# Kernel optimization log

Hardware: AMD Instinct MI355X
Metric: run time of the kernel (lower is better)

## Reference

```python
import jax, jax.numpy as jnp
import numpy as np

NUM_HEADS = 16
HEAD_DIM = 80
HIDDEN = 1280
SEQ = 3072
NUM_SEGS = 6  # 6 packed images of 512 patches each


def rotate_half(x):
    x1, x2 = jnp.split(x, 2, axis=-1)
    return jnp.concatenate([-x2, x1], axis=-1)


def setup_inputs() -> dict:
    key = jax.random.key(0)
    ks = jax.random.split(key, 6)
    hidden_states = jax.random.normal(ks[0], (SEQ, HIDDEN), dtype=jnp.float32)
    # RoPE tables as in Qwen-VL vision: freqs over half the head_dim, duplicated
    half = HEAD_DIM // 2
    inv_freq = 1.0 / (10000.0 ** (jnp.arange(half, dtype=jnp.float32) / half))
    pos = jnp.arange(SEQ, dtype=jnp.float32)[:, None]
    freqs = pos * inv_freq[None, :]                      # (SEQ, half)
    emb = jnp.concatenate([freqs, freqs], axis=-1)       # (SEQ, HEAD_DIM)
    cos = jnp.cos(emb)
    sin = jnp.sin(emb)
    # Packed segment boundaries: [0, 512, 1024, ..., 3072]
    cu_seqlens = jnp.arange(0, SEQ + 1, SEQ // NUM_SEGS, dtype=jnp.int32)
    scale = 0.02
    w_qkv = jax.random.normal(ks[1], (3 * HIDDEN, HIDDEN), dtype=jnp.float32) * scale
    b_qkv = jax.random.normal(ks[2], (3 * HIDDEN,), dtype=jnp.float32) * scale
    w_proj = jax.random.normal(ks[3], (HIDDEN, HIDDEN), dtype=jnp.float32) * scale
    b_proj = jax.random.normal(ks[4], (HIDDEN,), dtype=jnp.float32) * scale
    return {
        "hidden_states": hidden_states, "cos": cos, "sin": sin,
        "w_qkv": w_qkv, "b_qkv": b_qkv, "w_proj": w_proj, "b_proj": b_proj,
        "cu_seqlens": cu_seqlens,
    }


def reference(hidden_states, cos, sin, w_qkv, b_qkv, w_proj, b_proj, cu_seqlens):
    S, H = hidden_states.shape
    nh, hd = NUM_HEADS, H // NUM_HEADS

    # Fused QKV projection: (S, 3H) -> q, k, v each (S, nh, hd)
    qkv = hidden_states @ w_qkv.T + b_qkv
    qkv = qkv.reshape(S, 3, nh, hd)
    q, k, v = qkv[:, 0], qkv[:, 1], qkv[:, 2]

    # Inline RoPE on q/k (cos/sin broadcast over heads)
    c = cos[:, None, :]
    s = sin[:, None, :]
    q = q * c + rotate_half(q) * s
    k = k * c + rotate_half(k) * s

    # Original casts fp32 -> fp16 for the flash attention kernel
    q16 = q.astype(jnp.float16)
    k16 = k.astype(jnp.float16)
    v16 = v.astype(jnp.float16)

    # Varlen masking: tokens attend only within their own packed segment
    tok = jnp.arange(S)
    seg = jnp.searchsorted(cu_seqlens, tok, side="right")  # (S,)
    same_seg = seg[:, None] == seg[None, :]                 # (S, S)

    scale = hd ** (-0.5)
    # Scores accumulated in fp32 (as flash attention does internally)
    scores = jnp.einsum("qhd,khd->hqk", q16, k16,
                        preferred_element_type=jnp.float32) * scale
    scores = jnp.where(same_seg[None], scores, jnp.finfo(jnp.float32).min)
    weights = jax.nn.softmax(scores, axis=-1).astype(jnp.float16)  # (nh, S, S)

    attn = jnp.einsum("hqk,khd->qhd", weights, v16)  # (S, nh, hd) fp16
    attn = attn.astype(jnp.float32).reshape(S, H)
    return attn @ w_proj.T + b_proj
```

## Files before the change

### kernel.cpp

```cpp
#include <hip/hip_runtime.h>

typedef _Float16 f16;
typedef _Float16 half8 __attribute__((ext_vector_type(8)));
typedef _Float16 half4 __attribute__((ext_vector_type(4)));
typedef float f32x4 __attribute__((ext_vector_type(4)));

__device__ __forceinline__ void gld_lds16(const void* g, void* l) {
  __builtin_amdgcn_global_load_lds((const __attribute__((address_space(1))) void*)g,
                                   (__attribute__((address_space(3))) void*)l, 16, 0, 0);
}

template <int CTRL>
__device__ __forceinline__ float dppf(float x) {
  return __builtin_bit_cast(float,
      __builtin_amdgcn_mov_dpp(__builtin_bit_cast(int, x), CTRL, 0xf, 0xf, true));
}
__device__ __forceinline__ float dpp_max16(float v) {
  v = fmaxf(v, dppf<0xB1>(v));
  v = fmaxf(v, dppf<0x4E>(v));
  v = fmaxf(v, dppf<0x128>(v));
  v = fmaxf(v, dppf<0x140>(v));
  return v;
}
__device__ __forceinline__ float dpp_sum16(float v) {
  v += dppf<0xB1>(v);
  v += dppf<0x4E>(v);
  v += dppf<0x128>(v);
  v += dppf<0x140>(v);
  return v;
}

__global__ void cvt_all(const float* __restrict__ hid, const float* __restrict__ wq,
                        const float* __restrict__ wp, f16* __restrict__ hid16,
                        f16* __restrict__ wq16, f16* __restrict__ wp16) {
  int b = blockIdx.x;
  const float* in;
  f16* out;
  int i;
  if (b < 3840) { in = hid; out = hid16; i = b * 256 + threadIdx.x; }
  else if (b < 8640) { in = wq; out = wq16; i = (b - 3840) * 256 + threadIdx.x; }
  else { in = wp; out = wp16; i = (b - 8640) * 256 + threadIdx.x; }
  float4 v = ((const float4*)in)[i];
  half4 o;
  o.x = (f16)v.x; o.y = (f16)v.y; o.z = (f16)v.z; o.w = (f16)v.w;
  ((half4*)out)[i] = o;
}

__global__ __launch_bounds__(512, 2) void gemm240(const f16* __restrict__ A,
                                                  const f16* __restrict__ B,
                                                  const float* __restrict__ bias,
                                                  f16* __restrict__ C) {
  __shared__ f16 S[57344];
  char* Sb = (char*)S;
  const int tid = threadIdx.x, lane = tid & 63, wid = tid >> 6;
  const int lm = lane & 15, q4 = lane >> 4;
  const int wm = wid >> 2, wn = wid & 3;
  const int swz = ((int)blockIdx.x & 7) * 30 + ((int)blockIdx.x >> 3);
  const int bm = (swz % 12) * 256, bn = (swz / 12) * 192;

  const int ch = ((lane & 7) ^ (lane >> 3)) << 3;
  uint32_t aoff[4], boff[3];
#pragma unroll
  for (int q = 0; q < 4; q++)
    aoff[q] = (uint32_t)((bm + q * 64 + wid * 8 + (lane >> 3)) * 1280 + ch);
#pragma unroll
  for (int i = 0; i < 3; i++)
    boff[i] = (uint32_t)((bn + wid * 24 + i * 8 + (lane >> 3)) * 1280 + ch);

  const int xr = (lm & 7) << 4;
  int aro[2][2], bro[3][2];
#pragma unroll
  for (int f = 0; f < 2; f++)
#pragma unroll
    for (int ks = 0; ks < 2; ks++)
      aro[f][ks] = (wm * 32 + f * 16 + lm) * 128 + ((ks * 64 + q4 * 16) ^ xr);
#pragma unroll
  for (int nh = 0; nh < 3; nh++)
#pragma unroll
    for (int ks = 0; ks < 2; ks++)
      bro[nh][ks] = (nh * 64 + wn * 16 + lm) * 128 + ((ks * 64 + q4 * 16) ^ xr);

  f32x4 acc[8][3] = {};

  {
#pragma unroll
    for (int q = 0; q < 4; q++)
      gld_lds16(A + aoff[q], Sb + q * 8192 + wid * 1024);
#pragma unroll
    for (int i = 0; i < 3; i++)
      gld_lds16(B + boff[i], Sb + 65536 + (3 * wid + i) * 1024);
#pragma unroll
    for (int i = 0; i < 3; i++)
      gld_lds16(B + boff[i] + 64, Sb + 65536 + 24576 + (3 * wid + i) * 1024);
#pragma unroll
    for (int q = 0; q < 3; q++)
      gld_lds16(A + aoff[q] + 64, Sb + 32768 + q * 8192 + wid * 1024);
    asm volatile("s_waitcnt vmcnt(6)" ::: "memory");
    __builtin_amdgcn_s_barrier();
  }

  constexpr int NT = 20;
  half8 af[2][2], bf[3][2];
  for (int t = 0; t < NT; ++t) {
    const int p = t & 1;
    char* Ab = Sb + p * 32768;
    char* Bb = Sb + 65536 + p * 24576;
    const int k1 = (t + 1 < NT ? t + 1 : NT - 1) * 64;
    const int k2 = (t + 2 < NT ? t + 2 : NT - 1) * 64;

#pragma unroll
    for (int f = 0; f < 2; f++) {
      af[f][0] = *(const half8*)(Ab + aro[f][0]);
      af[f][1] = *(const half8*)(Ab + aro[f][1]);
    }
#pragma unroll
    for (int nh = 0; nh < 3; nh++) {
      bf[nh][0] = *(const half8*)(Bb + bro[nh][0]);
      bf[nh][1] = *(const half8*)(Bb + bro[nh][1]);
    }
    gld_lds16(A + aoff[3] + k1, Sb + (p ^ 1) * 32768 + 3 * 8192 + wid * 1024);
    __builtin_amdgcn_s_barrier();
    asm volatile("s_waitcnt lgkmcnt(0)" ::: "memory");
    __builtin_amdgcn_sched_barrier(0);
    __builtin_amdgcn_s_setprio(1);
#pragma unroll
    for (int ks = 0; ks < 2; ks++)
#pragma unroll
      for (int f = 0; f < 2; f++)
#pragma unroll
        for (int nh = 0; nh < 3; nh++)
          acc[f][nh] =
              __builtin_amdgcn_mfma_f32_16x16x32_f16(af[f][ks], bf[nh][ks], acc[f][nh], 0, 0, 0);
    __builtin_amdgcn_s_setprio(0);
    __builtin_amdgcn_s_barrier();

#pragma unroll
    for (int f = 0; f < 2; f++) {
      af[f][0] = *(const half8*)(Ab + 8192 + aro[f][0]);
      af[f][1] = *(const half8*)(Ab + 8192 + aro[f][1]);
    }
#pragma unroll
    for (int i = 0; i < 3; i++)
      gld_lds16(B + boff[i] + k2, Bb + (3 * wid + i) * 1024);
    gld_lds16(A + aoff[0] + k2, Ab + wid * 1024);
    __builtin_amdgcn_s_barrier();
    asm volatile("s_waitcnt lgkmcnt(0)" ::: "memory");
    __builtin_amdgcn_sched_barrier(0);
    __builtin_amdgcn_s_setprio(1);
#pragma unroll
    for (int ks = 0; ks < 2; ks++)
#pragma unroll
      for (int f = 0; f < 2; f++)
#pragma unroll
        for (int nh = 0; nh < 3; nh++)
          acc[2 + f][nh] = __builtin_amdgcn_mfma_f32_16x16x32_f16(af[f][ks], bf[nh][ks],
                                                                  acc[2 + f][nh], 0, 0, 0);
    __builtin_amdgcn_s_setprio(0);
    __builtin_amdgcn_s_barrier();

#pragma unroll
    for (int f = 0; f < 2; f++) {
      af[f][0] = *(const half8*)(Ab + 16384 + aro[f][0]);
      af[f][1] = *(const half8*)(Ab + 16384 + aro[f][1]);
    }
    gld_lds16(A + aoff[1] + k2, Ab + 8192 + wid * 1024);
    __builtin_amdgcn_s_barrier();
    asm volatile("s_waitcnt lgkmcnt(0)" ::: "memory");
    __builtin_amdgcn_sched_barrier(0);
    __builtin_amdgcn_s_setprio(1);
#pragma unroll
    for (int ks = 0; ks < 2; ks++)
#pragma unroll
      for (int f = 0; f < 2; f++)
#pragma unroll
        for (int nh = 0; nh < 3; nh++)
          acc[4 + f][nh] = __builtin_amdgcn_mfma_f32_16x16x32_f16(af[f][ks], bf[nh][ks],
                                                                  acc[4 + f][nh], 0, 0, 0);
    __builtin_amdgcn_s_setprio(0);
    __builtin_amdgcn_s_barrier();

#pragma unroll
    for (int f = 0; f < 2; f++) {
      af[f][0] = *(const half8*)(Ab + 24576 + aro[f][0]);
      af[f][1] = *(const half8*)(Ab + 24576 + aro[f][1]);
    }
    gld_lds16(A + aoff[2] + k2, Ab + 16384 + wid * 1024);
    asm volatile("s_waitcnt vmcnt(6)" ::: "memory");
    __builtin_amdgcn_s_barrier();
    asm volatile("s_waitcnt lgkmcnt(0)" ::: "memory");
    __builtin_amdgcn_sched_barrier(0);
    __builtin_amdgcn_s_setprio(1);
#pragma unroll
    for (int ks = 0; ks < 2; ks++)
#pragma unroll
      for (int f = 0; f < 2; f++)
#pragma unroll
        for (int nh = 0; nh < 3; nh++)
          acc[6 + f][nh] = __builtin_amdgcn_mfma_f32_16x16x32_f16(af[f][ks], bf[nh][ks],
                                                                  acc[6 + f][nh], 0, 0, 0);
    __builtin_amdgcn_s_setprio(0);
    __builtin_amdgcn_s_barrier();
  }

#pragma unroll
  for (int mf = 0; mf < 8; mf++)
#pragma unroll
    for (int nf = 0; nf < 3; nf++) {
      const int gc = bn + nf * 64 + wn * 16 + lm;
      const float bb = bias[gc];
      const int gr0 = bm + (mf >> 1) * 64 + wm * 32 + (mf & 1) * 16 + q4 * 4;
#pragma unroll
      for (int r = 0; r < 4; r++)
        C[(size_t)(gr0 + r) * 3840 + gc] = (f16)(acc[mf][nf][r] + bb);
    }
}

template <bool OUT_F16>
__global__ __launch_bounds__(256, 2) void gemm_bt64(const f16* __restrict__ A,
                                                    const f16* __restrict__ B,
                                                    const float* __restrict__ bias,
                                                    void* __restrict__ Cout,
                                                    int K, int lda, int ldb, int ldc) {
  __shared__ f16 As[64 * 32];
  __shared__ f16 Bs[128 * 32];
  const int tid = threadIdx.x, lane = tid & 63, wave = tid >> 6;
  const int bm = blockIdx.x * 64, bn = blockIdx.y * 128;
  const int wm = (wave & 1) * 32, wn = (wave >> 1) * 64;
  const int lm = lane & 15, kq = (lane >> 4) * 8;
  const int arow = tid >> 2, acol = (tid & 3) * 8;

  const f16* Ab = A + (size_t)(bm + arow) * lda + acol;
  const f16* Bb = B + (size_t)(bn + arow) * ldb + acol;
  f16* AsW = As + wave * 512;
  f16* BsW = Bs + wave * 512;

  f32x4 acc[2][4] = {};
  for (int k0 = 0; k0 < K; k0 += 32) {
    gld_lds16(Ab + k0, AsW);
    gld_lds16(Bb + k0, BsW);
    gld_lds16(Bb + (size_t)64 * ldb + k0, BsW + 2048);
    __syncthreads();
    half8 af[2], bf[4];
#pragma unroll
    for (int mt = 0; mt < 2; mt++) af[mt] = *(const half8*)&As[(wm + 16 * mt + lm) * 32 + kq];
#pragma unroll
    for (int nt = 0; nt < 4; nt++) bf[nt] = *(const half8*)&Bs[(wn + 16 * nt + lm) * 32 + kq];
#pragma unroll
    for (int mt = 0; mt < 2; mt++)
#pragma unroll
      for (int nt = 0; nt < 4; nt++)
        acc[mt][nt] = __builtin_amdgcn_mfma_f32_16x16x32_f16(af[mt], bf[nt], acc[mt][nt], 0, 0, 0);
    __syncthreads();
  }
  const int q4 = lane >> 4;
#pragma unroll
  for (int mt = 0; mt < 2; mt++)
#pragma unroll
    for (int nt = 0; nt < 4; nt++)
#pragma unroll
      for (int r = 0; r < 4; r++) {
        int gr = bm + wm + 16 * mt + 4 * q4 + r;
        int gc = bn + wn + 16 * nt + lm;
        float v = acc[mt][nt][r] + bias[gc];
        if (OUT_F16)
          ((f16*)Cout)[(size_t)gr * ldc + gc] = (f16)v;
        else
          ((float*)Cout)[(size_t)gr * ldc + gc] = v;
      }
}

__global__ void rope_transpose(f16* __restrict__ qkv, const float* __restrict__ cosb,
                               const float* __restrict__ sinb, f16* __restrict__ vt) {
  __shared__ f16 tile[64][72];
  const int b = blockIdx.x;
  if (b < 1920) {
    int idx = b * 256 + threadIdx.x;
    int c = idx % 5;
    int t = idx / 5;
    int h = t % 16; t /= 16;
    int qk = t & 1;
    int s = t >> 1;
    size_t base = (size_t)s * 3840 + qk * 1280 + h * 80 + c * 8;
    half8 x = *(half8*)&qkv[base];
    half8 y = *(half8*)&qkv[base + 40];
    const float* cp = cosb + s * 80 + c * 8;
    const float* sp = sinb + s * 80 + c * 8;
    half8 ox, oy;
#pragma unroll
    for (int i = 0; i < 8; i++) {
      float cs = cp[i], sn = sp[i];
      float xf = (float)x[i], yf = (float)y[i];
      ox[i] = (f16)(xf * cs - yf * sn);
      oy[i] = (f16)(yf * cs + xf * sn);
    }
    *(half8*)&qkv[base] = ox;
    *(half8*)&qkv[base + 40] = oy;
  } else {
    const int bb = b - 1920;
    const int bs = (bb % 48) * 64;
    const int bd = (bb / 48) * 64;
    const int r = threadIdx.x >> 2, c = (threadIdx.x & 3) * 16;
    *(uint4*)&tile[r][c] = *(const uint4*)&qkv[(size_t)(bs + r) * 3840 + 2560 + bd + c];
    *(uint4*)&tile[r][c + 8] = *(const uint4*)&qkv[(size_t)(bs + r) * 3840 + 2560 + bd + c + 8];
    __syncthreads();
    f16 tmp[16];
#pragma unroll
    for (int i = 0; i < 16; i++) tmp[i] = tile[c + i][r];
    *(uint4*)&vt[(size_t)(bd + r) * 3072 + bs + c] = *(uint4*)&tmp[0];
    *(uint4*)&vt[(size_t)(bd + r) * 3072 + bs + c + 8] = *(uint4*)&tmp[8];
  }
}

__global__ __launch_bounds__(256, 3) void flash_attn6(const f16* __restrict__ qkv,
                                                      const f16* __restrict__ vt,
                                                      f16* __restrict__ attn) {
  __shared__ f16 S[25088];
  const int tid = threadIdx.x, lane = tid & 63, wave = tid >> 6;
  const int lm = lane & 15, q4 = lane >> 4;
  const int h = blockIdx.x, g = blockIdx.z;
  const int qbase = g * 512 + blockIdx.y * 64 + wave * 16;
  f16* P = S + 20480 + wave * 1152;
  const half8 hz = {};

  const f16* qrow = qkv + (size_t)(qbase + lm) * 3840 + h * 80;
  half8 qf[3];
  qf[0] = *(const half8*)(qrow + q4 * 8);
  qf[1] = *(const half8*)(qrow + 32 + q4 * 8);
  qf[2] = (q4 < 2) ? *(const half8*)(qrow + 64 + q4 * 8) : hz;

  const bool isK = wave < 2;
  const f16* gsrc = isK ? qkv : vt;
  const uint32_t gstep = isK ? (uint32_t)(64 * 3840) : 64u;
  const int cbase = (wave & 1) * 5;
  const uint32_t ldsoff = (isK ? 0u : 5120u) + (uint32_t)cbase * 512u;
  uint32_t goff[5];
#pragma unroll
  for (int i = 0; i < 5; i++) {
    int t = (cbase + i) * 1024 + lane * 16;
    if (isK) {
      int row = t / 160, colb = t % 160;
      goff[i] = (uint32_t)((g * 512 + row) * 3840 + 1280 + h * 80 + (colb >> 1));
    } else {
      int vd = t >> 7, vsb = t & 127;
      int vsrc = vsb ^ ((vd & 7) << 4);
      goff[i] = (uint32_t)((h * 80 + vd) * 3072 + g * 512 + (vsrc >> 1));
    }
  }

  f32x4 oacc[5] = {};
  float mprev[4] = {-1e30f, -1e30f, -1e30f, -1e30f};
  float lsum[4] = {0.f, 0.f, 0.f, 0.f};
  const float sc = 0.11180339887498949f * 1.4426950408889634f;

#pragma unroll
  for (int i = 0; i < 5; i++) gld_lds16(gsrc + goff[i], S + ldsoff + i * 512);
  __syncthreads();

  for (int jj = 0; jj < 8; jj++) {
    const int p = jj & 1;
    f16* Kb = S + p * 10240;
    f16* Vb = Kb + 5120;
    if (jj < 7) {
#pragma unroll
      for (int i = 0; i < 5; i++)
        gld_lds16(gsrc + goff[i] + (uint32_t)(jj + 1) * gstep,
                  S + (p ^ 1) * 10240 + ldsoff + i * 512);
    }

    f32x4 sacc[4] = {};
#pragma unroll
    for (int ks = 0; ks < 3; ks++) {
      half8 bk[4];
#pragma unroll
      for (int nt = 0; nt < 4; nt++)
        bk[nt] = (ks < 2 || q4 < 2)
                     ? *(const half8*)&Kb[(16 * nt + lm) * 80 + 32 * ks + q4 * 8]
                     : hz;
#pragma unroll
      for (int nt = 0; nt < 4; nt++)
        sacc[nt] = __builtin_amdgcn_mfma_f32_16x16x32_f16(qf[ks], bk[nt], sacc[nt], 0, 0, 0);
    }

    float mnew[4], alpha[4], rs[4];
#pragma unroll
    for (int r = 0; r < 4; r++) {
      float v = fmaxf(fmaxf(sacc[0][r], sacc[1][r]), fmaxf(sacc[2][r], sacc[3][r]));
      v = dpp_max16(v);
      mnew[r] = fmaxf(mprev[r], v * sc);
      alpha[r] = __builtin_exp2f(mprev[r] - mnew[r]);
      mprev[r] = mnew[r];
      rs[r] = 0.f;
    }
#pragma unroll
    for (int nt = 0; nt < 4; nt++)
#pragma unroll
      for (int r = 0; r < 4; r++) {
        float pp = __builtin_exp2f(sacc[nt][r] * sc - mnew[r]);
        sacc[nt][r] = pp;
        rs[r] += pp;
      }
#pragma unroll
    for (int r = 0; r < 4; r++) {
      float v = dpp_sum16(rs[r]);
      lsum[r] = alpha[r] * lsum[r] + v;
#pragma unroll
      for (int nt2 = 0; nt2 < 5; nt2++) oacc[nt2][r] *= alpha[r];
    }

#pragma unroll
    for (int nt = 0; nt < 4; nt++)
#pragma unroll
      for (int r = 0; r < 4; r++)
        P[(4 * q4 + r) * 72 + 16 * nt + lm] = (f16)sacc[nt][r];

#pragma unroll
    for (int ks = 0; ks < 2; ks++) {
      half8 ap = *(const half8*)&P[lm * 72 + ks * 32 + q4 * 8];
      half8 bv[5];
#pragma unroll
      for (int nt2 = 0; nt2 < 5; nt2++) {
        int row = 16 * nt2 + lm;
        bv[nt2] = *(const half8*)&Vb[row * 64 + ((ks * 32 + q4 * 8) ^ ((row & 7) << 3))];
      }
#pragma unroll
      for (int nt2 = 0; nt2 < 5; nt2++)
        oacc[nt2] = __builtin_amdgcn_mfma_f32_16x16x32_f16(ap, bv[nt2], oacc[nt2], 0, 0, 0);
    }

    __syncthreads();
  }

#pragma unroll
  for (int r = 0; r < 4; r++) {
    float inv = 1.0f / lsum[r];
    int s = qbase + 4 * q4 + r;
#pragma unroll
    for (int nt2 = 0; nt2 < 5; nt2++)
      attn[(size_t)s * 1280 + h * 80 + 16 * nt2 + lm] = (f16)(oacc[nt2][r] * inv);
  }
}

extern "C" void kernel_launch(void* const* d_in, const int* in_sizes, int n_in,
                              void* d_out, int out_size, void* d_ws, size_t ws_size,
                              hipStream_t stream) {
  const float* hidden = (const float*)d_in[0];
  const float* cosb   = (const float*)d_in[1];
  const float* sinb   = (const float*)d_in[2];
  const float* w_qkv  = (const float*)d_in[3];
  const float* b_qkv  = (const float*)d_in[4];
  const float* w_proj = (const float*)d_in[5];
  const float* b_proj = (const float*)d_in[6];

  char* ws = (char*)d_ws;
  f16* hidden16 = (f16*)(ws + 0);
  f16* wqkv16   = (f16*)(ws + 7864320);
  f16* wproj16  = (f16*)(ws + 17694720);
  f16* qkv16    = (f16*)(ws + 20971520);
  f16* attn16   = (f16*)(ws + 44564480);
  f16* vt16     = hidden16;

  cvt_all<<<10240, 256, 0, stream>>>(hidden, w_qkv, w_proj, hidden16, wqkv16, wproj16);

  gemm240<<<240, 512, 0, stream>>>(hidden16, wqkv16, b_qkv, qkv16);

  rope_transpose<<<2880, 256, 0, stream>>>(qkv16, cosb, sinb, vt16);

  flash_attn6<<<dim3(16, 8, 6), 256, 0, stream>>>(qkv16, vt16, attn16);

  gemm_bt64<false><<<dim3(48, 10), 256, 0, stream>>>(attn16, wproj16, b_proj, d_out,
                                                     1280, 1280, 1280, 1280);
}
```

Baseline: 189.3 us.

## Restructure QKV GEMM main loop into two phases with fewer barriers

The QKV projection GEMM inner loop goes from four barrier-separated phases, each loading one A quarter, to two phases that each load two A quarters and issue twice as many MFMAs. The global-to-LDS prefetch order and vmcnt thresholds are reshuffled to match, and the prologue prefetch order changes. The aim is to halve the barriers and waits per k-tile and give each MFMA burst more work. In exchange it holds more A fragments in registers, which may raise register pressure at the 2-blocks-per-CU launch bound. It also relies on the new prefetch/wait ordering staying correct.

```diff
diff --git a/kernel.cpp b/kernel.cpp
--- a/kernel.cpp
+++ b/kernel.cpp
@@ -89,116 +89,84 @@
 #pragma unroll
     for (int i = 0; i < 3; i++)
       gld_lds16(B + boff[i], Sb + 65536 + (3 * wid + i) * 1024);
+    gld_lds16(A + aoff[0] + 64, Sb + 32768 + wid * 1024);
+    gld_lds16(A + aoff[1] + 64, Sb + 32768 + 8192 + wid * 1024);
 #pragma unroll
     for (int i = 0; i < 3; i++)
       gld_lds16(B + boff[i] + 64, Sb + 65536 + 24576 + (3 * wid + i) * 1024);
-#pragma unroll
-    for (int q = 0; q < 3; q++)
-      gld_lds16(A + aoff[q] + 64, Sb + 32768 + q * 8192 + wid * 1024);
-    asm volatile("s_waitcnt vmcnt(6)" ::: "memory");
+    asm volatile("s_waitcnt vmcnt(5)" ::: "memory");
     __builtin_amdgcn_s_barrier();
   }
 
   constexpr int NT = 20;
-  half8 af[2][2], bf[3][2];
   for (int t = 0; t < NT; ++t) {
     const int p = t & 1;
     char* Ab = Sb + p * 32768;
     char* Bb = Sb + 65536 + p * 24576;
+    char* An = Sb + (p ^ 1) * 32768;
     const int k1 = (t + 1 < NT ? t + 1 : NT - 1) * 64;
     const int k2 = (t + 2 < NT ? t + 2 : NT - 1) * 64;
 
-#pragma unroll
-    for (int f = 0; f < 2; f++) {
-      af[f][0] = *(const half8*)(Ab + aro[f][0]);
-      af[f][1] = *(const half8*)(Ab + aro[f][1]);
-    }
-#pragma unroll
-    for (int nh = 0; nh < 3; nh++) {
-      bf[nh][0] = *(const half8*)(Bb + bro[nh][0]);
-      bf[nh][1] = *(const half8*)(Bb + bro[nh][1]);
-    }
-    gld_lds16(A + aoff[3] + k1, Sb + (p ^ 1) * 32768 + 3 * 8192 + wid * 1024);
+    half8 a0[2][2], a1[2][2], bf[3][2];
+#pragma unroll
+    for (int f = 0; f < 2; f++)
+#pragma unroll
+      for (int ks = 0; ks < 2; ks++) {
+        a0[f][ks] = *(const half8*)(Ab + aro[f][ks]);
+        a1[f][ks] = *(const half8*)(Ab + 8192 + aro[f][ks]);
+      }
+#pragma unroll
+    for (int nh = 0; nh < 3; nh++)
+#pragma unroll
+      for (int ks = 0; ks < 2; ks++)
+        bf[nh][ks] = *(const half8*)(Bb + bro[nh][ks]);
+    gld_lds16(A + aoff[2] + k1, An + 2 * 8192 + wid * 1024);
+    gld_lds16(A + aoff[3] + k1, An + 3 * 8192 + wid * 1024);
+    __builtin_amdgcn_s_setprio(1);
+#pragma unroll
+    for (int ks = 0; ks < 2; ks++)
+#pragma unroll
+      for (int f = 0; f < 2; f++)
+#pragma unroll
+        for (int nh = 0; nh < 3; nh++) {
+          acc[f][nh] =
+              __builtin_amdgcn_mfma_f32_16x16x32_f16(a0[f][ks], bf[nh][ks], acc[f][nh], 0, 0, 0);
+          acc[2 + f][nh] = __builtin_amdgcn_mfma_f32_16x16x32_f16(a1[f][ks], bf[nh][ks],
+                                                                  acc[2 + f][nh], 0, 0, 0);
+        }
+    __builtin_amdgcn_s_setprio(0);
+    __builtin_amdgcn_sched_barrier(0);
+    asm volatile("s_waitcnt lgkmcnt(0)" ::: "memory");
     __builtin_amdgcn_s_barrier();
-    asm volatile("s_waitcnt lgkmcnt(0)" ::: "memory");
-    __builtin_amdgcn_sched_barrier(0);
-    __builtin_amdgcn_s_setprio(1);
-#pragma unroll
-    for (int ks = 0; ks < 2; ks++)
-#pragma unroll
-      for (int f = 0; f < 2; f++)
-#pragma unroll
-        for (int nh = 0; nh < 3; nh++)
-          acc[f][nh] =
-              __builtin_amdgcn_mfma_f32_16x16x32_f16(af[f][ks], bf[nh][ks], acc[f][nh], 0, 0, 0);
-    __builtin_amdgcn_s_setprio(0);
-    __builtin_amdgcn_s_barrier();
-
-#pragma unroll
-    for (int f = 0; f < 2; f++) {
-      af[f][0] = *(const half8*)(Ab + 8192 + aro[f][0]);
-      af[f][1] = *(const half8*)(Ab + 8192 + aro[f][1]);
-    }
+
+#pragma unroll
+    for (int f = 0; f < 2; f++)
+#pragma unroll
+      for (int ks = 0; ks < 2; ks++) {
+        a0[f][ks] = *(const half8*)(Ab + 16384 + aro[f][ks]);
+        a1[f][ks] = *(const half8*)(Ab + 24576 + aro[f][ks]);
+      }
+    gld_lds16(A + aoff[0] + k2, Ab + wid * 1024);
+    gld_lds16(A + aoff[1] + k2, Ab + 8192 + wid * 1024);
 #pragma unroll
     for (int i = 0; i < 3; i++)
       gld_lds16(B + boff[i] + k2, Bb + (3 * wid + i) * 1024);
-    gld_lds16(A + aoff[0] + k2, Ab + wid * 1024);
-    __builtin_amdgcn_s_barrier();
+    __builtin_amdgcn_s_setprio(1);
+#pragma unroll
+    for (int ks = 0; ks < 2; ks++)
+#pragma unroll
+      for (int f = 0; f < 2; f++)
+#pragma unroll
+        for (int nh = 0; nh < 3; nh++) {
+          acc[4 + f][nh] = __builtin_amdgcn_mfma_f32_16x16x32_f16(a0[f][ks], bf[nh][ks],
+                                                                  acc[4 + f][nh], 0, 0, 0);
+          acc[6 + f][nh] = __builtin_amdgcn_mfma_f32_16x16x32_f16(a1[f][ks], bf[nh][ks],
+                                                                  acc[6 + f][nh], 0, 0, 0);
+        }
+    __builtin_amdgcn_s_setprio(0);
+    __builtin_amdgcn_sched_barrier(0);
+    asm volatile("s_waitcnt vmcnt(5)" ::: "memory");
     asm volatile("s_waitcnt lgkmcnt(0)" ::: "memory");
-    __builtin_amdgcn_sched_barrier(0);
-    __builtin_amdgcn_s_setprio(1);
-#pragma unroll
-    for (int ks = 0; ks < 2; ks++)
-#pragma unroll
-      for (int f = 0; f < 2; f++)
-#pragma unroll
-        for (int nh = 0; nh < 3; nh++)
-          acc[2 + f][nh] = __builtin_amdgcn_mfma_f32_16x16x32_f16(af[f][ks], bf[nh][ks],
-                                                                  acc[2 + f][nh], 0, 0, 0);
-    __builtin_amdgcn_s_setprio(0);
-    __builtin_amdgcn_s_barrier();
-
-#pragma unroll
-    for (int f = 0; f < 2; f++) {
-      af[f][0] = *(const half8*)(Ab + 16384 + aro[f][0]);
-      af[f][1] = *(const half8*)(Ab + 16384 + aro[f][1]);
-    }
-    gld_lds16(A + aoff[1] + k2, Ab + 8192 + wid * 1024);
-    __builtin_amdgcn_s_barrier();
-    asm volatile("s_waitcnt lgkmcnt(0)" ::: "memory");
-    __builtin_amdgcn_sched_barrier(0);
-    __builtin_amdgcn_s_setprio(1);
-#pragma unroll
-    for (int ks = 0; ks < 2; ks++)
-#pragma unroll
-      for (int f = 0; f < 2; f++)
-#pragma unroll
-        for (int nh = 0; nh < 3; nh++)
-          acc[4 + f][nh] = __builtin_amdgcn_mfma_f32_16x16x32_f16(af[f][ks], bf[nh][ks],
-                                                                  acc[4 + f][nh], 0, 0, 0);
-    __builtin_amdgcn_s_setprio(0);
-    __builtin_amdgcn_s_barrier();
-
-#pragma unroll
-    for (int f = 0; f < 2; f++) {
-      af[f][0] = *(const half8*)(Ab + 24576 + aro[f][0]);
-      af[f][1] = *(const half8*)(Ab + 24576 + aro[f][1]);
-    }
-    gld_lds16(A + aoff[2] + k2, Ab + 16384 + wid * 1024);
-    asm volatile("s_waitcnt vmcnt(6)" ::: "memory");
-    __builtin_amdgcn_s_barrier();
-    asm volatile("s_waitcnt lgkmcnt(0)" ::: "memory");
-    __builtin_amdgcn_sched_barrier(0);
-    __builtin_amdgcn_s_setprio(1);
-#pragma unroll
-    for (int ks = 0; ks < 2; ks++)
-#pragma unroll
-      for (int f = 0; f < 2; f++)
-#pragma unroll
-        for (int nh = 0; nh < 3; nh++)
-          acc[6 + f][nh] = __builtin_amdgcn_mfma_f32_16x16x32_f16(af[f][ks], bf[nh][ks],
-                                                                  acc[6 + f][nh], 0, 0, 0);
-    __builtin_amdgcn_s_setprio(0);
     __builtin_amdgcn_s_barrier();
   }
 
```

Measured after the change: 189.0 us. About the same (-0.2%).
